# Kernel optimization log

Measured on AMD Instinct MI355X. Metric: run time of the kernel, lower is better.

## Reference

```python
import jax, jax.numpy as jnp
import numpy as np

# Model dims
P_SPECS = [(6, 256), (7, 256)]          # pattern_length -> num_patterns (ordered)
P = 512                                  # total_num_patterns
MAXL = 7                                 # max_pattern_length
ND = 2                                   # num_diags (self-loop diag + main diag)
D = 300                                  # embedding_dim
V = 50000                                # vocab size
B = 32                                   # batch size
T = 128                                  # max_doc_len
NC = 2                                   # num_classes
NEG = -1e30                              # max-sum semiring zero; one = 0.0
END_STATES = np.concatenate([np.full(n, l - 1, dtype=np.int32) for l, n in P_SPECS])


def setup_inputs() -> dict:
    key = jax.random.key(0)
    ks = jax.random.split(key, 8)
    tokens = jax.random.randint(ks[0], (B, T), 0, V, dtype=jnp.int32)
    doc_lens = jax.random.randint(ks[1], (B,), 64, T + 1, dtype=jnp.int32)
    emb_table = jax.random.normal(ks[2], (V, D), dtype=jnp.float32)
    diags = jax.random.normal(ks[3], (P * ND * MAXL, D), dtype=jnp.float32)
    diags = diags / jnp.linalg.norm(diags, axis=1, keepdims=True)  # normalize(diags)
    bias = jax.random.normal(ks[4], (P * ND * MAXL, 1), dtype=jnp.float32)
    epsilons = jax.random.normal(ks[5], (P, MAXL - 1), dtype=jnp.float32)
    bn_weight = jnp.ones((P,), jnp.float32)
    bn_bias = jnp.zeros((P,), jnp.float32)
    final_w = 0.05 * jax.random.normal(ks[6], (NC, P), dtype=jnp.float32)
    final_b = jnp.zeros((NC,), jnp.float32)
    return dict(tokens=tokens, doc_lens=doc_lens, emb_table=emb_table, diags=diags,
                bias=bias, epsilons=epsilons, bn_weight=bn_weight, bn_bias=bn_bias,
                final_w=final_w, final_b=final_b)


def reference(tokens, doc_lens, emb_table, diags, bias, epsilons,
              bn_weight, bn_bias, final_w, final_b):
    # --- transition matrices (max-sum semiring: from_outer is identity) ---
    emb = emb_table[tokens]                                   # [B,T,D]
    # mm(diags, embeddings) + bias_scale * bias  (bias_scale = 1.0)
    ts = jnp.einsum('btd,kd->btk', emb, diags) + bias[:, 0]   # [B,T,P*ND*MAXL]
    ts = ts.reshape(B, T, P, ND, MAXL)                        # [B,T,P,ND,MAXL]

    end = jnp.asarray(END_STATES)                             # [P]
    hid0 = jnp.full((B, P, MAXL), NEG, jnp.float32).at[:, :, 0].set(0.0)
    sc0 = jnp.full((B, P), NEG, jnp.float32)                  # semiring.zero
    zpad = jnp.full((B, P, 1), NEG, jnp.float32)              # zero_padding
    rpad = jnp.zeros((B, P, 1), jnp.float32)                  # restart_padding (one)

    # epsilon_values = epsilon_scale (one=0) + epsilons
    def step(carry, xs):
        hid, sc = carry
        tm, i = xs                                            # tm: [B,P,ND,MAXL]
        # epsilon transitions
        ae = jnp.maximum(hid, jnp.concatenate([zpad, hid[:, :, :-1] + epsilons], axis=2))
        # main path: diag index -1 (the main diagonal)
        main = jnp.concatenate([rpad, ae[:, :, :-1] + tm[:, :, -1, :-1]], axis=2)
        # self loops: diag 0, self_loop_scale = semiring.one = 0
        sl = ae + tm[:, :, 0, :]
        hid = jnp.maximum(main, sl)
        endv = jnp.take_along_axis(hid, jnp.broadcast_to(end[None, :, None], (B, P, 1)), axis=2)[:, :, 0]
        sc = jnp.where((doc_lens > i)[:, None], jnp.maximum(sc, endv), sc)
        return (hid, sc), None

    (_, scores), _ = jax.lax.scan(step, (hid0, sc0),
                                  (jnp.moveaxis(ts, 1, 0), jnp.arange(T, dtype=jnp.int32)))

    # BatchNorm1d (training mode: biased batch statistics)
    mean = scores.mean(axis=0)
    var = scores.var(axis=0)
    scores = (scores - mean) * jax.lax.rsqrt(var + 1e-5) * bn_weight + bn_bias
    # binarize_scores
    scores = jnp.sign(jax.nn.relu(scores))
    # final linear layer
    return scores @ final_w.T + final_b                       # [B, NC]
```

## Files before the change

kernel.cpp:

```cpp
#include <hip/hip_runtime.h>

#define BB 32
#define TT 128
#define PP 512
#define DD 300
#define KP 320
#define NR 13
#define NN 6656
#define NEG -1e30f

typedef _Float16 half8 __attribute__((ext_vector_type(8)));
typedef _Float16 half4 __attribute__((ext_vector_type(4)));
typedef float floatx4 __attribute__((ext_vector_type(4)));

__device__ __forceinline__ void async_load16(const void* g, void* l) {
    __builtin_amdgcn_global_load_lds(
        (const __attribute__((address_space(1))) void*)g,
        (__attribute__((address_space(3))) void*)l, 16, 0, 0);
}

__device__ __forceinline__ floatx4 mfma16(half8 a, half8 b, floatx4 c) {
    return __builtin_amdgcn_mfma_f32_16x16x32_f16(a, b, c, 0, 0, 0);
}

__global__ __launch_bounds__(256) void pack_kernel(
    const int* __restrict__ tokens, const float* __restrict__ emb,
    const float* __restrict__ diags, const float* __restrict__ bias,
    _Float16* __restrict__ Ah, _Float16* __restrict__ Al,
    _Float16* __restrict__ Bh, _Float16* __restrict__ Bl)
{
    const int idx = blockIdx.x * 256 + threadIdx.x;
    if (idx >= (4096 + NN) * 80) return;
    const int r = idx / 80;
    const int c = idx - r * 80;

    float4 x = make_float4(0.f, 0.f, 0.f, 0.f);
    float4 xl_extra = make_float4(0.f, 0.f, 0.f, 0.f);
    _Float16* dh;
    _Float16* dl;

    if (r < 4096) {
        if (c < 75) x = *(const float4*)(emb + (size_t)tokens[r] * DD + c * 4);
        else if (c == 75) x.x = 1.0f;
        dh = Ah + (size_t)r * KP + c * 4;
        dl = Al + (size_t)r * KP + c * 4;
    } else {
        const int n = r - 4096;
        const int p = n / NR;
        const int rr = n - p * NR;
        const int srow = p * 14 + rr;
        if (c < 75) x = *(const float4*)(diags + (size_t)srow * DD + c * 4);
        else if (c == 75) x.x = bias[srow];
        dh = Bh + (size_t)n * KP + c * 4;
        dl = Bl + (size_t)n * KP + c * 4;
    }

    half4 h, l;
    h.x = (_Float16)x.x; l.x = (_Float16)((x.x - (float)h.x) * 4096.f);
    h.y = (_Float16)x.y; l.y = (_Float16)((x.y - (float)h.y) * 4096.f);
    h.z = (_Float16)x.z; l.z = (_Float16)((x.z - (float)h.z) * 4096.f);
    h.w = (_Float16)x.w; l.w = (_Float16)((x.w - (float)h.w) * 4096.f);
    if (r < 4096 && c == 75) { l.x = (_Float16)0.f; }
    (void)xl_extra;
    *(half4*)dh = h;
    *(half4*)dl = l;
}

__global__ __launch_bounds__(256, 2) void gemm_kernel(
    const _Float16* __restrict__ Ah, const _Float16* __restrict__ Al,
    const _Float16* __restrict__ Bh, const _Float16* __restrict__ Bl,
    float* __restrict__ C)
{
    __shared__ __align__(16) _Float16 AsH[2][128 * 32];
    __shared__ __align__(16) _Float16 AsL[2][128 * 32];
    __shared__ __align__(16) _Float16 BsH[2][128 * 32];
    __shared__ __align__(16) _Float16 BsL[2][128 * 32];

    const int tid = threadIdx.x;
    const int w = tid >> 6, ln = tid & 63;
    const int n0 = blockIdx.x * 128, m0 = blockIdx.y * 128;
    const int wm = w & 1, wn = w >> 1;

    floatx4 acc0[4][4], acc1[4][4];
    #pragma unroll
    for (int i = 0; i < 4; ++i)
        #pragma unroll
        for (int j = 0; j < 4; ++j) {
            acc0[i][j] = (floatx4){0.f, 0.f, 0.f, 0.f};
            acc1[i][j] = (floatx4){0.f, 0.f, 0.f, 0.f};
        }

    const int srow = ln >> 2;
    const int sch  = (ln & 3) * 8;
    const int fr = ln & 15;
    const int kg = ln >> 4;

    const _Float16* gsrc = (w == 0) ? Ah + (size_t)m0 * KP
                        : (w == 1) ? Al + (size_t)m0 * KP
                        : (w == 2) ? Bh + (size_t)n0 * KP
                                   : Bl + (size_t)n0 * KP;
    _Float16* lbase = (w == 0) ? &AsH[0][0]
                    : (w == 1) ? &AsL[0][0]
                    : (w == 2) ? &BsH[0][0]
                               : &BsL[0][0];

    for (int kt = 0; kt < KP / 64; ++kt) {
        const int k0 = kt * 64;
        #pragma unroll
        for (int kb = 0; kb < 2; ++kb) {
            #pragma unroll
            for (int s = 0; s < 8; ++s) {
                async_load16(gsrc + (size_t)(s * 16 + srow) * KP + k0 + kb * 32 + sch,
                             lbase + kb * (128 * 32) + s * 16 * 32);
            }
        }
        __syncthreads();

        #pragma unroll
        for (int kb = 0; kb < 2; ++kb) {
            half8 ah4[4], al4[4];
            #pragma unroll
            for (int i = 0; i < 4; ++i) {
                const int off = (wm * 64 + i * 16 + fr) * 32 + kg * 8;
                ah4[i] = *(const half8*)&AsH[kb][off];
                al4[i] = *(const half8*)&AsL[kb][off];
            }
            #pragma unroll
            for (int j = 0; j < 4; ++j) {
                const int off = (wn * 64 + j * 16 + fr) * 32 + kg * 8;
                const half8 bh = *(const half8*)&BsH[kb][off];
                const half8 bl = *(const half8*)&BsL[kb][off];
                #pragma unroll
                for (int i = 0; i < 4; ++i) {
                    acc0[i][j] = mfma16(ah4[i], bh, acc0[i][j]);
                    acc1[i][j] = mfma16(ah4[i], bl, acc1[i][j]);
                    acc1[i][j] = mfma16(al4[i], bh, acc1[i][j]);
                }
            }
        }
        __syncthreads();
    }

    #pragma unroll
    for (int j = 0; j < 4; ++j) {
        const int n = n0 + wn * 64 + j * 16 + fr;
        #pragma unroll
        for (int i = 0; i < 4; ++i) {
            const int mb = m0 + wm * 64 + i * 16 + kg * 4;
            #pragma unroll
            for (int r = 0; r < 4; ++r)
                C[(size_t)(mb + r) * NN + n] =
                    acc0[i][j][r] + acc1[i][j][r] * (1.0f / 4096.0f);
        }
    }
}

__global__ __launch_bounds__(64) void scan_kernel(
    const float* __restrict__ ts,
    const float* __restrict__ epsilons,
    const int* __restrict__ doc_lens,
    float* __restrict__ scores)
{
    const int b = blockIdx.x;
    const int p = blockIdx.y * 64 + threadIdx.x;
    const int dl = doc_lens[b];

    float e[6];
    #pragma unroll
    for (int i = 0; i < 6; ++i) e[i] = epsilons[p * 6 + i];

    const float* base = ts + (size_t)b * TT * NN + p * NR;

    float h0 = 0.f, h1 = NEG, h2 = NEG, h3 = NEG, h4 = NEG, h5 = NEG, h6 = NEG;
    float sc = NEG;
    const bool end5 = (p < 256);

    float v0[NR], v1[NR];

    auto load = [&](float* v, int t) {
        const float* s = base + (size_t)t * NN;
        #pragma unroll
        for (int i = 0; i < NR; ++i) v[i] = s[i];
    };
    auto step = [&](const float* v, int t) {
        float ae0 = h0;
        float ae1 = fmaxf(h1, h0 + e[0]);
        float ae2 = fmaxf(h2, h1 + e[1]);
        float ae3 = fmaxf(h3, h2 + e[2]);
        float ae4 = fmaxf(h4, h3 + e[3]);
        float ae5 = fmaxf(h5, h4 + e[4]);
        float ae6 = fmaxf(h6, h5 + e[5]);
        h0 = fmaxf(0.f,          ae0 + v[0]);
        h1 = fmaxf(ae0 + v[7],   ae1 + v[1]);
        h2 = fmaxf(ae1 + v[8],   ae2 + v[2]);
        h3 = fmaxf(ae2 + v[9],   ae3 + v[3]);
        h4 = fmaxf(ae3 + v[10],  ae4 + v[4]);
        h5 = fmaxf(ae4 + v[11],  ae5 + v[5]);
        h6 = fmaxf(ae5 + v[12],  ae6 + v[6]);
        const float endv = end5 ? h5 : h6;
        if (t < dl) sc = fmaxf(sc, endv);
    };

    load(v0, 0);
    for (int t = 0; t < TT - 2; t += 2) {
        load(v1, t + 1);
        step(v0, t);
        load(v0, t + 2);
        step(v1, t + 1);
    }
    load(v1, TT - 1);
    step(v0, TT - 2);
    step(v1, TT - 1);

    scores[p * BB + b] = sc;
}

__global__ __launch_bounds__(512) void finalize_kernel(
    const float* __restrict__ scores,
    const float* __restrict__ bn_w,
    const float* __restrict__ bn_b,
    const float* __restrict__ fw,
    const float* __restrict__ fb,
    float* __restrict__ out)
{
    __shared__ float acc[64];
    const int p = threadIdx.x;
    if (p < 64) acc[p] = 0.f;
    __syncthreads();

    float x[32];
    const float4* sp = (const float4*)(scores + p * 32);
    #pragma unroll
    for (int i = 0; i < 8; ++i) ((float4*)x)[i] = sp[i];

    float mean = 0.f;
    #pragma unroll
    for (int i = 0; i < 32; ++i) mean += x[i];
    mean *= (1.f / 32.f);
    float var = 0.f;
    #pragma unroll
    for (int i = 0; i < 32; ++i) { const float d = x[i] - mean; var = fmaf(d, d, var); }
    var *= (1.f / 32.f);

    const float scale = (1.f / sqrtf(var + 1e-5f)) * bn_w[p];
    const float shift = bn_b[p];
    const float w0 = fw[p], w1 = fw[PP + p];

    for (int b = 0; b < 32; ++b) {
        const float v = (x[b] - mean) * scale + shift;
        const bool bin = v > 0.f;
        float v0 = bin ? w0 : 0.f;
        float v1 = bin ? w1 : 0.f;
        #pragma unroll
        for (int o = 32; o; o >>= 1) {
            v0 += __shfl_xor(v0, o);
            v1 += __shfl_xor(v1, o);
        }
        if ((threadIdx.x & 63) == 0) {
            atomicAdd(&acc[b * 2 + 0], v0);
            atomicAdd(&acc[b * 2 + 1], v1);
        }
    }
    __syncthreads();
    if (p < 64) out[p] = acc[p] + fb[p & 1];
}

extern "C" void kernel_launch(void* const* d_in, const int* in_sizes, int n_in,
                              void* d_out, int out_size, void* d_ws, size_t ws_size,
                              hipStream_t stream) {
    const int*   tokens   = (const int*)d_in[0];
    const int*   doc_lens = (const int*)d_in[1];
    const float* emb      = (const float*)d_in[2];
    const float* diags    = (const float*)d_in[3];
    const float* bias     = (const float*)d_in[4];
    const float* eps      = (const float*)d_in[5];
    const float* bnw      = (const float*)d_in[6];
    const float* bnb      = (const float*)d_in[7];
    const float* fw       = (const float*)d_in[8];
    const float* fb       = (const float*)d_in[9];
    float* out = (float*)d_out;

    float* ts     = (float*)d_ws;
    float* scores = ts + (size_t)4096 * NN;
    _Float16* Ah  = (_Float16*)(scores + PP * BB);
    _Float16* Al  = Ah + (size_t)4096 * KP;
    _Float16* Bh  = Al + (size_t)4096 * KP;
    _Float16* Bl  = Bh + (size_t)NN * KP;

    pack_kernel<<<((4096 + NN) * 80 + 255) / 256, 256, 0, stream>>>(
        tokens, emb, diags, bias, Ah, Al, Bh, Bl);
    gemm_kernel<<<dim3(NN / 128, 32), 256, 0, stream>>>(Ah, Al, Bh, Bl, ts);
    scan_kernel<<<dim3(32, 8), 64, 0, stream>>>(ts, eps, doc_lens, scores);
    finalize_kernel<<<1, 512, 0, stream>>>(scores, bnw, bnb, fw, fb, out);
}
```

Measured before the change: 214.3 us.

## Pad per-pattern transition rows to 14 floats and deepen scan prefetch

The GEMM epilogue now writes each pattern's 13 transition values into a 14-float padded slot, giving a row stride of 7168. This lets the scan kernel read them as aligned float2 vectors. The scan also switches from double buffering to a 4-deep rotating prefetch, so more loads are in flight during the latency-bound recurrence. In exchange the intermediate buffer grows by about 8%, and the GEMM stores become slightly less regular because of the per-column division by 13.

```diff
diff --git a/kernel.cpp b/kernel.cpp
--- a/kernel.cpp
+++ b/kernel.cpp
@@ -7,6 +7,7 @@
 #define KP 320
 #define NR 13
 #define NN 6656
+#define NS 7168
 #define NEG -1e30f
 
 typedef _Float16 half8 __attribute__((ext_vector_type(8)));
@@ -35,7 +36,6 @@
     const int c = idx - r * 80;
 
     float4 x = make_float4(0.f, 0.f, 0.f, 0.f);
-    float4 xl_extra = make_float4(0.f, 0.f, 0.f, 0.f);
     _Float16* dh;
     _Float16* dl;
 
@@ -61,7 +61,6 @@
     h.z = (_Float16)x.z; l.z = (_Float16)((x.z - (float)h.z) * 4096.f);
     h.w = (_Float16)x.w; l.w = (_Float16)((x.w - (float)h.w) * 4096.f);
     if (r < 4096 && c == 75) { l.x = (_Float16)0.f; }
-    (void)xl_extra;
     *(half4*)dh = h;
     *(half4*)dl = l;
 }
@@ -144,12 +143,13 @@
     #pragma unroll
     for (int j = 0; j < 4; ++j) {
         const int n = n0 + wn * 64 + j * 16 + fr;
+        const int col = n + (unsigned)n / 13u;
         #pragma unroll
         for (int i = 0; i < 4; ++i) {
             const int mb = m0 + wm * 64 + i * 16 + kg * 4;
             #pragma unroll
             for (int r = 0; r < 4; ++r)
-                C[(size_t)(mb + r) * NN + n] =
+                C[(size_t)(mb + r) * NS + col] =
                     acc0[i][j][r] + acc1[i][j][r] * (1.0f / 4096.0f);
         }
     }
@@ -169,20 +169,21 @@
     #pragma unroll
     for (int i = 0; i < 6; ++i) e[i] = epsilons[p * 6 + i];
 
-    const float* base = ts + (size_t)b * TT * NN + p * NR;
+    const float* base = ts + (size_t)b * TT * NS + p * 14;
 
     float h0 = 0.f, h1 = NEG, h2 = NEG, h3 = NEG, h4 = NEG, h5 = NEG, h6 = NEG;
     float sc = NEG;
     const bool end5 = (p < 256);
 
-    float v0[NR], v1[NR];
-
-    auto load = [&](float* v, int t) {
-        const float* s = base + (size_t)t * NN;
-        #pragma unroll
-        for (int i = 0; i < NR; ++i) v[i] = s[i];
+    float2 buf[4][7];
+
+    auto load = [&](int slot, int t) {
+        const float2* s = (const float2*)(base + (size_t)t * NS);
+        #pragma unroll
+        for (int i = 0; i < 7; ++i) buf[slot][i] = s[i];
     };
-    auto step = [&](const float* v, int t) {
+    auto step = [&](int slot, int t) {
+        const float2* v = buf[slot];
         float ae0 = h0;
         float ae1 = fmaxf(h1, h0 + e[0]);
         float ae2 = fmaxf(h2, h1 + e[1]);
@@ -190,27 +191,29 @@
         float ae4 = fmaxf(h4, h3 + e[3]);
         float ae5 = fmaxf(h5, h4 + e[4]);
         float ae6 = fmaxf(h6, h5 + e[5]);
-        h0 = fmaxf(0.f,          ae0 + v[0]);
-        h1 = fmaxf(ae0 + v[7],   ae1 + v[1]);
-        h2 = fmaxf(ae1 + v[8],   ae2 + v[2]);
-        h3 = fmaxf(ae2 + v[9],   ae3 + v[3]);
-        h4 = fmaxf(ae3 + v[10],  ae4 + v[4]);
-        h5 = fmaxf(ae4 + v[11],  ae5 + v[5]);
-        h6 = fmaxf(ae5 + v[12],  ae6 + v[6]);
+        h0 = fmaxf(0.f,            ae0 + v[0].x);
+        h1 = fmaxf(ae0 + v[3].y,   ae1 + v[0].y);
+        h2 = fmaxf(ae1 + v[4].x,   ae2 + v[1].x);
+        h3 = fmaxf(ae2 + v[4].y,   ae3 + v[1].y);
+        h4 = fmaxf(ae3 + v[5].x,   ae4 + v[2].x);
+        h5 = fmaxf(ae4 + v[5].y,   ae5 + v[2].y);
+        h6 = fmaxf(ae5 + v[6].x,   ae6 + v[3].x);
         const float endv = end5 ? h5 : h6;
         if (t < dl) sc = fmaxf(sc, endv);
     };
 
-    load(v0, 0);
-    for (int t = 0; t < TT - 2; t += 2) {
-        load(v1, t + 1);
-        step(v0, t);
-        load(v0, t + 2);
-        step(v1, t + 1);
-    }
-    load(v1, TT - 1);
-    step(v0, TT - 2);
-    step(v1, TT - 1);
+    #pragma unroll
+    for (int j = 0; j < 4; ++j) load(j, j);
+
+    for (int tb = 0; tb < TT - 4; tb += 4) {
+        #pragma unroll
+        for (int j = 0; j < 4; ++j) {
+            step(j, tb + j);
+            load(j, tb + j + 4);
+        }
+    }
+    #pragma unroll
+    for (int j = 0; j < 4; ++j) step(j, TT - 4 + j);
 
     scores[p * BB + b] = sc;
 }
@@ -281,7 +284,7 @@
     float* out = (float*)d_out;
 
     float* ts     = (float*)d_ws;
-    float* scores = ts + (size_t)4096 * NN;
+    float* scores = ts + (size_t)4096 * NS;
     _Float16* Ah  = (_Float16*)(scores + PP * BB);
     _Float16* Al  = Ah + (size_t)4096 * KP;
     _Float16* Bh  = Al + (size_t)4096 * KP;
```

Result: slower. 223.5 us (+4.3%).
